# Kernel optimization log

Measured on AMD Instinct MI355X. Metric: run time of the kernel, lower is better.

The kernel has to match this reference:

```python
import jax, jax.numpy as jnp
import numpy as np

EPS = 1e-5


def setup_inputs() -> dict:
    key = jax.random.key(0)
    ks = jax.random.split(key, 6)
    B, N, F = 8, 8192, 64
    xyzs = jax.random.uniform(ks[0], (B, N, 3), dtype=jnp.float32)
    feats = jax.random.normal(ks[1], (B, N, F), dtype=jnp.float32)
    c_in = 3 + F  # 67
    dims = [(64, c_in), (64, 64), (128, 64)]
    inp = {"xyzs": xyzs, "feats": feats}
    for i, (co, ci) in enumerate(dims, start=1):
        inp[f"w{i}"] = jax.random.normal(ks[1 + i], (co, ci), dtype=jnp.float32) / np.sqrt(ci)
        inp[f"b{i}"] = jnp.zeros((co,), jnp.float32)
        inp[f"g{i}"] = jnp.ones((co,), jnp.float32)
        inp[f"bt{i}"] = jnp.zeros((co,), jnp.float32)
        inp[f"m{i}"] = jnp.zeros((co,), jnp.float32)
        inp[f"v{i}"] = jnp.ones((co,), jnp.float32)
    return inp


def sample_farthest_points(xyz, S):
    # Iterative FPS starting from index 0 (pytorch3d default random_start_point=False).
    B, N, _ = xyz.shape
    barange = jnp.arange(B)

    def step(carry, _):
        mind, last = carry                      # mind: [B,N] min sq-dist to selected set
        lastp = xyz[barange, last]              # [B,3]
        d = jnp.sum((xyz - lastp[:, None, :]) ** 2, -1)
        mind = jnp.minimum(mind, d)
        nxt = jnp.argmax(mind, axis=1).astype(jnp.int32)
        return (mind, nxt), nxt

    init = (jnp.full((B, N), 1e10, xyz.dtype), jnp.zeros((B,), jnp.int32))
    _, rest = jax.lax.scan(step, init, None, length=S - 1)  # [S-1, B]
    idx = jnp.concatenate([jnp.zeros((1, B), jnp.int32), rest], 0).T  # [B,S]
    return xyz[barange[:, None], idx], idx


def ball_query(centers, xyz, K, radius):
    # First-K-in-radius semantics of pytorch3d.ops.ball_query; pad idx with -1,
    # pad gathered points with zeros (masked_gather behavior).
    B, N, _ = xyz.shape
    d2 = (jnp.sum(centers ** 2, -1)[:, :, None]
          + jnp.sum(xyz ** 2, -1)[:, None, :]
          - 2.0 * jnp.einsum('bsd,bnd->bsn', centers, xyz))  # [B,S,N]
    within = d2 <= radius * radius
    skey = jnp.where(within, jnp.arange(N, dtype=jnp.int32), N)
    negvals, idx = jax.lax.top_k(-skey, K)      # K smallest keys = first K in-radius
    valid = (-negvals) < N                       # [B,S,K]
    group_idx = jnp.where(valid, idx, -1)
    gathered = xyz[jnp.arange(B)[:, None, None], jnp.where(valid, idx, 0)]  # [B,S,K,3]
    group_xyz = jnp.where(valid[..., None], gathered, 0.0)
    return group_idx, group_xyz


def _mlp_layer(x, w, b, g, bt, m, v):
    # 1x1 Conv2d over channel axis + BatchNorm (eval stats) + ReLU; x: [B,S,K,Cin]
    y = jnp.einsum('bskc,oc->bsko', x, w) + b
    y = g * (y - m) * jax.lax.rsqrt(v + EPS) + bt
    return jax.nn.relu(y)


def reference(xyzs, feats, w1, b1, g1, bt1, m1, v1,
              w2, b2, g2, bt2, m2, v2, w3, b3, g3, bt3, m3, v3):
    S, K, radius = 2048, 32, 0.2
    B = xyzs.shape[0]
    center_xyzs, _ = sample_farthest_points(xyzs, S)             # [B,S,3]
    group_idxs, group_xyzs = ball_query(center_xyzs, xyzs, K, radius)
    group_xyzs = group_xyzs - center_xyzs[:, :, None, :]          # relative coords
    batch_idxs = jnp.arange(B)[:, None, None]
    gf = feats[batch_idxs, jnp.where(group_idxs < 0, 0, group_idxs)]  # [B,S,K,F]
    gf = jnp.concatenate([group_xyzs, gf], axis=-1)
    gf = gf * (group_idxs != -1)[..., None].astype(gf.dtype)      # zero padded slots
    x = _mlp_layer(gf, w1, b1, g1, bt1, m1, v1)
    x = _mlp_layer(x, w2, b2, g2, bt2, m2, v2)
    x = _mlp_layer(x, w3, b3, g3, bt3, m3, v3)
    center_feats = jnp.max(x, axis=2)                             # max over neighbors
    return center_xyzs, center_feats
```

## Files before the change

kernel.cpp:

```cpp
#include <hip/hip_runtime.h>


#define NPTS 8192
#define SCTR 2048
#define NB   8
#define KNN  32
#define NF   64

typedef float v2f __attribute__((ext_vector_type(2)));

__device__ __forceinline__ v2f fps_sqdist_v2(v2f px, v2f py, v2f pz,
                                             v2f lx, v2f ly, v2f lz) {
#pragma clang fp contract(off)
  v2f dx = px - lx;
  v2f dy = py - ly;
  v2f dz = pz - lz;
  v2f xx = dx * dx;
  v2f yy = dy * dy;
  v2f zz = dz * dz;
  return (xx + yy) + zz;
}

__device__ __forceinline__ float sumsq3(float x, float y, float z) {
#pragma clang fp contract(off)
  return (x * x + y * y) + z * z;
}

__device__ __forceinline__ float bq_d2(float sc, float sx,
                                       float cx, float cy, float cz,
                                       float x, float y, float z) {
#pragma clang fp contract(off)
  float dt = fmaf(cz, z, fmaf(cy, y, cx * x));
  return (sc + sx) - 2.0f * dt;
}

template <int CTRL>
__device__ __forceinline__ unsigned long long kmax_dpp(unsigned long long k) {
  int lo = (int)(unsigned int)(k & 0xFFFFFFFFull);
  int hi = (int)(unsigned int)(k >> 32);
  int slo = __builtin_amdgcn_update_dpp(lo, lo, CTRL, 0xF, 0xF, false);
  int shi = __builtin_amdgcn_update_dpp(hi, hi, CTRL, 0xF, 0xF, false);
  unsigned long long sk =
      ((unsigned long long)(unsigned int)shi << 32) | (unsigned int)slo;
  return sk > k ? sk : k;
}

__global__ __launch_bounds__(256, 1) void fps_transpose_kernel(
    const float* __restrict__ xyzs,
    const float* __restrict__ w1, const float* __restrict__ w2, const float* __restrict__ w3,
    float* __restrict__ centers, float* __restrict__ wT)
{
  const int t = threadIdx.x;
  if (blockIdx.x >= NB) {
    int idx = (blockIdx.x - NB) * 256 + t;
    if (idx < 67*64) {
      int c = idx >> 6, o = idx & 63;
      wT[idx] = w1[o*67 + c];
    } else if (idx < 67*64 + 64*64) {
      int r = idx - 67*64; int c = r >> 6, o = r & 63;
      wT[idx] = w2[o*64 + c];
    } else if (idx < 67*64 + 64*64 + 64*128) {
      int r = idx - (67*64 + 64*64); int c = r >> 7, o = r & 127;
      wT[idx] = w3[o*64 + c];
    }
    return;
  }

  const int b = blockIdx.x;
  const float* xb = xyzs + (size_t)b * NPTS * 3;

  __shared__ float sX[NPTS], sY[NPTS], sZ[NPTS];
  __shared__ unsigned long long redk[2][4];
  __shared__ int hist[SCTR];

  for (int i = t; i < NPTS; i += 256) {
    sX[i] = xb[3*i+0];
    sY[i] = xb[3*i+1];
    sZ[i] = xb[3*i+2];
  }
  if (t == 0) hist[0] = 0;
  __syncthreads();

  const int t4 = 4 * t;

  const float4 xA = *(const float4*)(sX + 0    + t4);
  const float4 yA = *(const float4*)(sY + 0    + t4);
  const float4 zA = *(const float4*)(sZ + 0    + t4);
  const float4 xB = *(const float4*)(sX + 1024 + t4);
  const float4 yB = *(const float4*)(sY + 1024 + t4);
  const float4 zB = *(const float4*)(sZ + 1024 + t4);
  const float4 xC = *(const float4*)(sX + 2048 + t4);
  const float4 yC = *(const float4*)(sY + 2048 + t4);
  const float4 zC = *(const float4*)(sZ + 2048 + t4);
  const float4 xD = *(const float4*)(sX + 3072 + t4);
  const float4 yD = *(const float4*)(sY + 3072 + t4);
  const float4 zD = *(const float4*)(sZ + 3072 + t4);
  const float4 xE = *(const float4*)(sX + 4096 + t4);
  const float4 yE = *(const float4*)(sY + 4096 + t4);
  const float4 zE = *(const float4*)(sZ + 4096 + t4);
  const float4 xF = *(const float4*)(sX + 5120 + t4);
  const float4 yF = *(const float4*)(sY + 5120 + t4);
  const float4 zF = *(const float4*)(sZ + 5120 + t4);
  const float4 xG = *(const float4*)(sX + 6144 + t4);
  const float4 yG = *(const float4*)(sY + 6144 + t4);
  const float4 zG = *(const float4*)(sZ + 6144 + t4);
  const float4 xH = *(const float4*)(sX + 7168 + t4);
  const float4 yH = *(const float4*)(sY + 7168 + t4);
  const float4 zH = *(const float4*)(sZ + 7168 + t4);

  float4 mA = make_float4(1e10f,1e10f,1e10f,1e10f);
  float4 mB = mA, mC = mA, mD = mA, mE = mA, mF = mA, mG = mA, mH = mA;

  float lx = sX[0], ly = sY[0], lz = sZ[0];

#define FPS_QUAD(QX, QY, QZ, MV, QOFF, BV, BG)                                  \
  do {                                                                          \
    v2f d;                                                                      \
    d = fps_sqdist_v2((v2f){QX.x,QX.y}, (v2f){QY.x,QY.y}, (v2f){QZ.x,QZ.y},     \
                      lxv, lyv, lzv);                                           \
    MV.x = fminf(MV.x, d.x); if (MV.x > BV) { BV = MV.x; BG = (QOFF)+t4+0; }    \
    MV.y = fminf(MV.y, d.y); if (MV.y > BV) { BV = MV.y; BG = (QOFF)+t4+1; }    \
    d = fps_sqdist_v2((v2f){QX.z,QX.w}, (v2f){QY.z,QY.w}, (v2f){QZ.z,QZ.w},     \
                      lxv, lyv, lzv);                                           \
    MV.z = fminf(MV.z, d.x); if (MV.z > BV) { BV = MV.z; BG = (QOFF)+t4+2; }    \
    MV.w = fminf(MV.w, d.y); if (MV.w > BV) { BV = MV.w; BG = (QOFF)+t4+3; }    \
  } while (0)

  for (int s = 1; s < SCTR; ++s) {
    float bv0 = -1.0f, bv1 = -1.0f; int bg0 = 0, bg1 = 0;
    {
      v2f lxv = {lx, lx}, lyv = {ly, ly}, lzv = {lz, lz};
      FPS_QUAD(xA, yA, zA, mA, 0,    bv0, bg0);
      FPS_QUAD(xB, yB, zB, mB, 1024, bv0, bg0);
      FPS_QUAD(xC, yC, zC, mC, 2048, bv0, bg0);
      FPS_QUAD(xD, yD, zD, mD, 3072, bv0, bg0);
      FPS_QUAD(xE, yE, zE, mE, 4096, bv1, bg1);
      FPS_QUAD(xF, yF, zF, mF, 5120, bv1, bg1);
      FPS_QUAD(xG, yG, zG, mG, 6144, bv1, bg1);
      FPS_QUAD(xH, yH, zH, mH, 7168, bv1, bg1);
    }
    float bv = bv0; int bg = bg0;
    if (bv1 > bv0) { bv = bv1; bg = bg1; }

    unsigned long long key =
        ((unsigned long long)__float_as_uint(bv) << 13) |
        (unsigned long long)(8191 - bg);

    key = kmax_dpp<0x111>(key);
    key = kmax_dpp<0x112>(key);
    key = kmax_dpp<0x114>(key);
    key = kmax_dpp<0x118>(key);
    key = kmax_dpp<0x142>(key);
    key = kmax_dpp<0x143>(key);

    int pb = s & 1;
    if ((t & 63) == 63) redk[pb][t >> 6] = key;
    __syncthreads();

    unsigned long long k4 = redk[pb][t & 3];
    k4 = kmax_dpp<0xB1>(k4);
    k4 = kmax_dpp<0x4E>(k4);

    int i0 = 8191 - (int)(k4 & 0x1FFFull);
    lx = sX[i0]; ly = sY[i0]; lz = sZ[i0];
    if (t == 0) hist[s] = i0;
  }
#undef FPS_QUAD
  __syncthreads();

  for (int s = t; s < SCTR; s += 256) {
    int i = hist[s];
    float* o = centers + ((size_t)b * SCTR + s) * 3;
    o[0] = sX[i]; o[1] = sY[i]; o[2] = sZ[i];
  }
}

__global__ __launch_bounds__(64) void sa_fused_kernel(
    const float* __restrict__ xyzs, const float* __restrict__ feats,
    const float* centers, const float* __restrict__ wT,
    const float* __restrict__ b1, const float* __restrict__ g1, const float* __restrict__ bt1,
    const float* __restrict__ m1, const float* __restrict__ v1,
    const float* __restrict__ b2, const float* __restrict__ g2, const float* __restrict__ bt2,
    const float* __restrict__ m2, const float* __restrict__ v2,
    const float* __restrict__ b3, const float* __restrict__ g3, const float* __restrict__ bt3,
    const float* __restrict__ m3, const float* __restrict__ v3,
    float* out_feats)
{
  constexpr float R2 = (float)(0.2 * 0.2);
  const int bid  = blockIdx.x;
  const int b    = bid >> 11;
  const int lane = threadIdx.x;
  const float* xb = xyzs + (size_t)b * NPTS * 3;
  const float* cp = centers + (size_t)bid * 3;
  float cx = cp[0], cy = cp[1], cz = cp[2];
  float sc = sumsq3(cx, cy, cz);

  __shared__ int   gidx[KNN];
  __shared__ float in_[32*67];
  __shared__ float y_[32*65];

  int cnt = 0;
  for (int base = 0; base < NPTS && cnt < KNN; base += 64) {
    int n = base + lane;
    float x = xb[n*3+0], y = xb[n*3+1], z = xb[n*3+2];
    float sx = sumsq3(x, y, z);
    float d2 = bq_d2(sc, sx, cx, cy, cz, x, y, z);
    bool within = (d2 <= R2);
    unsigned long long mk = __ballot(within);
    int rank = __popcll(mk & ((1ull << lane) - 1ull));
    int slot = cnt + rank;
    if (within && slot < KNN) gidx[slot] = n;
    cnt += (int)__popcll(mk);
  }
  if (cnt > KNN) cnt = KNN;
  __syncthreads();

#pragma unroll 4
  for (int k = 0; k < KNN; ++k) {
    int gk = (k < cnt) ? gidx[k] : -1;
    float fv = 0.f, xv = 0.f;
    if (gk >= 0) {
      fv = feats[((size_t)b * NPTS + gk) * NF + lane];
      if (lane < 3) xv = xb[gk*3 + lane] - cp[lane];
    }
    in_[k*67 + 3 + lane] = fv;
    if (lane < 3) in_[k*67 + lane] = xv;
  }
  __syncthreads();

  const int g = lane >> 3;
  const int h = lane & 7;
  const float* w1T = wT;
  const float* w2T = wT + 67*64;
  const float* w3T = wT + 67*64 + 64*64;

  {
    float acc[4][8];
#pragma unroll
    for (int i=0;i<4;++i)
#pragma unroll
      for (int j=0;j<8;++j) acc[i][j]=0.f;
#pragma unroll 4
    for (int c = 0; c < 67; ++c) {
      float a0 = in_[(4*g+0)*67 + c];
      float a1 = in_[(4*g+1)*67 + c];
      float a2 = in_[(4*g+2)*67 + c];
      float a3 = in_[(4*g+3)*67 + c];
      const float* wr = w1T + c*64 + 8*h;
      float4 wv0 = *(const float4*)(wr);
      float4 wv1 = *(const float4*)(wr + 4);
      float wj[8] = {wv0.x,wv0.y,wv0.z,wv0.w,wv1.x,wv1.y,wv1.z,wv1.w};
#pragma unroll
      for (int j=0;j<8;++j) {
        acc[0][j] = fmaf(a0, wj[j], acc[0][j]);
        acc[1][j] = fmaf(a1, wj[j], acc[1][j]);
        acc[2][j] = fmaf(a2, wj[j], acc[2][j]);
        acc[3][j] = fmaf(a3, wj[j], acc[3][j]);
      }
    }
    float scl[8], shf[8];
#pragma unroll
    for (int j=0;j<8;++j) {
      int o = 8*h + j;
      float r = g1[o] * rsqrtf(v1[o] + 1e-5f);
      scl[j] = r;
      shf[j] = (b1[o] - m1[o]) * r + bt1[o];
    }
#pragma unroll
    for (int i=0;i<4;++i) {
      int k = 4*g + i;
#pragma unroll
      for (int j=0;j<8;++j)
        y_[k*65 + 8*h + j] = fmaxf(fmaf(acc[i][j], scl[j], shf[j]), 0.f);
    }
  }
  __syncthreads();

  {
    float acc[4][8];
#pragma unroll
    for (int i=0;i<4;++i)
#pragma unroll
      for (int j=0;j<8;++j) acc[i][j]=0.f;
#pragma unroll 4
    for (int c = 0; c < 64; ++c) {
      float a0 = y_[(4*g+0)*65 + c];
      float a1 = y_[(4*g+1)*65 + c];
      float a2 = y_[(4*g+2)*65 + c];
      float a3 = y_[(4*g+3)*65 + c];
      const float* wr = w2T + c*64 + 8*h;
      float4 wv0 = *(const float4*)(wr);
      float4 wv1 = *(const float4*)(wr + 4);
      float wj[8] = {wv0.x,wv0.y,wv0.z,wv0.w,wv1.x,wv1.y,wv1.z,wv1.w};
#pragma unroll
      for (int j=0;j<8;++j) {
        acc[0][j] = fmaf(a0, wj[j], acc[0][j]);
        acc[1][j] = fmaf(a1, wj[j], acc[1][j]);
        acc[2][j] = fmaf(a2, wj[j], acc[2][j]);
        acc[3][j] = fmaf(a3, wj[j], acc[3][j]);
      }
    }
    float scl[8], shf[8];
#pragma unroll
    for (int j=0;j<8;++j) {
      int o = 8*h + j;
      float r = g2[o] * rsqrtf(v2[o] + 1e-5f);
      scl[j] = r;
      shf[j] = (b2[o] - m2[o]) * r + bt2[o];
    }
    __syncthreads();
#pragma unroll
    for (int i=0;i<4;++i) {
      int k = 4*g + i;
#pragma unroll
      for (int j=0;j<8;++j)
        in_[k*65 + 8*h + j] = fmaxf(fmaf(acc[i][j], scl[j], shf[j]), 0.f);
    }
  }
  __syncthreads();

  for (int p = 0; p < 2; ++p) {
    float acc[4][8];
#pragma unroll
    for (int i=0;i<4;++i)
#pragma unroll
      for (int j=0;j<8;++j) acc[i][j]=0.f;
#pragma unroll 4
    for (int c = 0; c < 64; ++c) {
      float a0 = in_[(4*g+0)*65 + c];
      float a1 = in_[(4*g+1)*65 + c];
      float a2 = in_[(4*g+2)*65 + c];
      float a3 = in_[(4*g+3)*65 + c];
      const float* wr = w3T + c*128 + p*64 + 8*h;
      float4 wv0 = *(const float4*)(wr);
      float4 wv1 = *(const float4*)(wr + 4);
      float wj[8] = {wv0.x,wv0.y,wv0.z,wv0.w,wv1.x,wv1.y,wv1.z,wv1.w};
#pragma unroll
      for (int j=0;j<8;++j) {
        acc[0][j] = fmaf(a0, wj[j], acc[0][j]);
        acc[1][j] = fmaf(a1, wj[j], acc[1][j]);
        acc[2][j] = fmaf(a2, wj[j], acc[2][j]);
        acc[3][j] = fmaf(a3, wj[j], acc[3][j]);
      }
    }
    float scl[8], shf[8];
#pragma unroll
    for (int j=0;j<8;++j) {
      int o = p*64 + 8*h + j;
      float r = g3[o] * rsqrtf(v3[o] + 1e-5f);
      scl[j] = r;
      shf[j] = (b3[o] - m3[o]) * r + bt3[o];
    }
    float vm[8];
#pragma unroll
    for (int j=0;j<8;++j) {
      float q0 = fmaxf(fmaf(acc[0][j], scl[j], shf[j]), 0.f);
      float q1 = fmaxf(fmaf(acc[1][j], scl[j], shf[j]), 0.f);
      float q2 = fmaxf(fmaf(acc[2][j], scl[j], shf[j]), 0.f);
      float q3 = fmaxf(fmaf(acc[3][j], scl[j], shf[j]), 0.f);
      vm[j] = fmaxf(fmaxf(q0,q1), fmaxf(q2,q3));
    }
#pragma unroll
    for (int mk = 8; mk < 64; mk <<= 1) {
#pragma unroll
      for (int j=0;j<8;++j) vm[j] = fmaxf(vm[j], __shfl_xor(vm[j], mk));
    }
    if (g == 0) {
      float* dst = out_feats + (size_t)bid*128 + p*64 + 8*h;
      *(float4*)dst       = make_float4(vm[0],vm[1],vm[2],vm[3]);
      *(float4*)(dst + 4) = make_float4(vm[4],vm[5],vm[6],vm[7]);
    }
  }
}

extern "C" void kernel_launch(void* const* d_in, const int* in_sizes, int n_in,
                              void* d_out, int out_size, void* d_ws, size_t ws_size,
                              hipStream_t stream) {
  const float* xyzs  = (const float*)d_in[0];
  const float* feats = (const float*)d_in[1];
  const float* w1  = (const float*)d_in[2];
  const float* b1  = (const float*)d_in[3];
  const float* g1  = (const float*)d_in[4];
  const float* bt1 = (const float*)d_in[5];
  const float* m1  = (const float*)d_in[6];
  const float* v1  = (const float*)d_in[7];
  const float* w2  = (const float*)d_in[8];
  const float* b2  = (const float*)d_in[9];
  const float* g2  = (const float*)d_in[10];
  const float* bt2 = (const float*)d_in[11];
  const float* m2  = (const float*)d_in[12];
  const float* v2  = (const float*)d_in[13];
  const float* w3  = (const float*)d_in[14];
  const float* b3  = (const float*)d_in[15];
  const float* g3  = (const float*)d_in[16];
  const float* bt3 = (const float*)d_in[17];
  const float* m3  = (const float*)d_in[18];
  const float* v3  = (const float*)d_in[19];

  float* out       = (float*)d_out;
  float* centers   = out;
  float* out_feats = out + (size_t)NB * SCTR * 3;
  float* wT        = (float*)d_ws;

  hipLaunchKernelGGL(fps_transpose_kernel, dim3(NB + 65), dim3(256), 0, stream,
                     xyzs, w1, w2, w3, centers, wT);
  hipLaunchKernelGGL(sa_fused_kernel, dim3(NB * SCTR), dim3(64), 0, stream,
                     xyzs, feats, centers, wT,
                     b1, g1, bt1, m1, v1,
                     b2, g2, bt2, m2, v2,
                     b3, g3, bt3, m3, v3,
                     out_feats);
}
```

Baseline: 2.362 ms.

## Split fused MLP across two waves and force packed FP32 ops in FPS

The fused ball-query and MLP kernel now runs 128 threads per center instead of 64. Each wave computes half of the output channels of every layer, and the feature gather is split across the two waves. The FPS distance update is rewritten with inline v_pk_add_f32 and v_pk_mul_f32, adding a negated last point so that packed FP32 instructions are guaranteed. The wider block shortens the per-thread dependent chain and cuts register use, at the cost of both waves running the ball-query scan redundantly; the inline asm also limits what the compiler can schedule.

```diff
diff --git a/kernel.cpp b/kernel.cpp
--- a/kernel.cpp
+++ b/kernel.cpp
@@ -9,16 +9,11 @@
 
 typedef float v2f __attribute__((ext_vector_type(2)));
 
-__device__ __forceinline__ v2f fps_sqdist_v2(v2f px, v2f py, v2f pz,
-                                             v2f lx, v2f ly, v2f lz) {
-#pragma clang fp contract(off)
-  v2f dx = px - lx;
-  v2f dy = py - ly;
-  v2f dz = pz - lz;
-  v2f xx = dx * dx;
-  v2f yy = dy * dy;
-  v2f zz = dz * dz;
-  return (xx + yy) + zz;
+__device__ __forceinline__ v2f pk_add(v2f a, v2f b) {
+  v2f r; asm("v_pk_add_f32 %0, %1, %2" : "=v"(r) : "v"(a), "v"(b)); return r;
+}
+__device__ __forceinline__ v2f pk_mul(v2f a, v2f b) {
+  v2f r; asm("v_pk_mul_f32 %0, %1, %2" : "=v"(r) : "v"(a), "v"(b)); return r;
 }
 
 __device__ __forceinline__ float sumsq3(float x, float y, float z) {
@@ -113,23 +108,30 @@
 
   float lx = sX[0], ly = sY[0], lz = sZ[0];
 
-#define FPS_QUAD(QX, QY, QZ, MV, QOFF, BV, BG)                                  \
-  do {                                                                          \
-    v2f d;                                                                      \
-    d = fps_sqdist_v2((v2f){QX.x,QX.y}, (v2f){QY.x,QY.y}, (v2f){QZ.x,QZ.y},     \
-                      lxv, lyv, lzv);                                           \
-    MV.x = fminf(MV.x, d.x); if (MV.x > BV) { BV = MV.x; BG = (QOFF)+t4+0; }    \
-    MV.y = fminf(MV.y, d.y); if (MV.y > BV) { BV = MV.y; BG = (QOFF)+t4+1; }    \
-    d = fps_sqdist_v2((v2f){QX.z,QX.w}, (v2f){QY.z,QY.w}, (v2f){QZ.z,QZ.w},     \
-                      lxv, lyv, lzv);                                           \
-    MV.z = fminf(MV.z, d.x); if (MV.z > BV) { BV = MV.z; BG = (QOFF)+t4+2; }    \
-    MV.w = fminf(MV.w, d.y); if (MV.w > BV) { BV = MV.w; BG = (QOFF)+t4+3; }    \
+#define FPS_HALF(PX0, PX1, PY0, PY1, PZ0, PZ1, MM0, MM1, I0, I1, BV, BG)     \
+  do {                                                                       \
+    v2f px_ = {PX0, PX1}, py_ = {PY0, PY1}, pz_ = {PZ0, PZ1};               \
+    v2f dx_ = pk_add(px_, nlx);                                              \
+    v2f dy_ = pk_add(py_, nly);                                              \
+    v2f dz_ = pk_add(pz_, nlz);                                              \
+    v2f dd_ = pk_add(pk_add(pk_mul(dx_,dx_), pk_mul(dy_,dy_)),               \
+                     pk_mul(dz_,dz_));                                       \
+    MM0 = fminf(MM0, dd_.x); if (MM0 > BV) { BV = MM0; BG = (I0); }          \
+    MM1 = fminf(MM1, dd_.y); if (MM1 > BV) { BV = MM1; BG = (I1); }          \
+  } while (0)
+
+#define FPS_QUAD(QX, QY, QZ, MV, QOFF, BV, BG)                               \
+  do {                                                                       \
+    FPS_HALF(QX.x, QX.y, QY.x, QY.y, QZ.x, QZ.y, MV.x, MV.y,                 \
+             (QOFF)+t4+0, (QOFF)+t4+1, BV, BG);                              \
+    FPS_HALF(QX.z, QX.w, QY.z, QY.w, QZ.z, QZ.w, MV.z, MV.w,                 \
+             (QOFF)+t4+2, (QOFF)+t4+3, BV, BG);                              \
   } while (0)
 
   for (int s = 1; s < SCTR; ++s) {
     float bv0 = -1.0f, bv1 = -1.0f; int bg0 = 0, bg1 = 0;
     {
-      v2f lxv = {lx, lx}, lyv = {ly, ly}, lzv = {lz, lz};
+      v2f nlx = {-lx, -lx}, nly = {-ly, -ly}, nlz = {-lz, -lz};
       FPS_QUAD(xA, yA, zA, mA, 0,    bv0, bg0);
       FPS_QUAD(xB, yB, zB, mB, 1024, bv0, bg0);
       FPS_QUAD(xC, yC, zC, mC, 2048, bv0, bg0);
@@ -166,6 +168,7 @@
     if (t == 0) hist[s] = i0;
   }
 #undef FPS_QUAD
+#undef FPS_HALF
   __syncthreads();
 
   for (int s = t; s < SCTR; s += 256) {
@@ -175,7 +178,7 @@
   }
 }
 
-__global__ __launch_bounds__(64) void sa_fused_kernel(
+__global__ __launch_bounds__(128) void sa_fused_kernel(
     const float* __restrict__ xyzs, const float* __restrict__ feats,
     const float* centers, const float* __restrict__ wT,
     const float* __restrict__ b1, const float* __restrict__ g1, const float* __restrict__ bt1,
@@ -189,7 +192,9 @@
   constexpr float R2 = (float)(0.2 * 0.2);
   const int bid  = blockIdx.x;
   const int b    = bid >> 11;
-  const int lane = threadIdx.x;
+  const int tid  = threadIdx.x;
+  const int w    = tid >> 6;
+  const int lane = tid & 63;
   const float* xb = xyzs + (size_t)b * NPTS * 3;
   const float* cp = centers + (size_t)bid * 3;
   float cx = cp[0], cy = cp[1], cz = cp[2];
@@ -216,7 +221,8 @@
   __syncthreads();
 
 #pragma unroll 4
-  for (int k = 0; k < KNN; ++k) {
+  for (int k2 = 0; k2 < 16; ++k2) {
+    int k = 2*k2 + w;
     int gk = (k < cnt) ? gidx[k] : -1;
     float fv = 0.f, xv = 0.f;
     if (gk >= 0) {
@@ -235,33 +241,31 @@
   const float* w3T = wT + 67*64 + 64*64;
 
   {
-    float acc[4][8];
+    float acc[4][4];
 #pragma unroll
     for (int i=0;i<4;++i)
 #pragma unroll
-      for (int j=0;j<8;++j) acc[i][j]=0.f;
+      for (int j=0;j<4;++j) acc[i][j]=0.f;
 #pragma unroll 4
     for (int c = 0; c < 67; ++c) {
       float a0 = in_[(4*g+0)*67 + c];
       float a1 = in_[(4*g+1)*67 + c];
       float a2 = in_[(4*g+2)*67 + c];
       float a3 = in_[(4*g+3)*67 + c];
-      const float* wr = w1T + c*64 + 8*h;
-      float4 wv0 = *(const float4*)(wr);
-      float4 wv1 = *(const float4*)(wr + 4);
-      float wj[8] = {wv0.x,wv0.y,wv0.z,wv0.w,wv1.x,wv1.y,wv1.z,wv1.w};
-#pragma unroll
-      for (int j=0;j<8;++j) {
+      float4 wv = *(const float4*)(w1T + c*64 + w*32 + 4*h);
+      float wj[4] = {wv.x, wv.y, wv.z, wv.w};
+#pragma unroll
+      for (int j=0;j<4;++j) {
         acc[0][j] = fmaf(a0, wj[j], acc[0][j]);
         acc[1][j] = fmaf(a1, wj[j], acc[1][j]);
         acc[2][j] = fmaf(a2, wj[j], acc[2][j]);
         acc[3][j] = fmaf(a3, wj[j], acc[3][j]);
       }
     }
-    float scl[8], shf[8];
-#pragma unroll
-    for (int j=0;j<8;++j) {
-      int o = 8*h + j;
+    float scl[4], shf[4];
+#pragma unroll
+    for (int j=0;j<4;++j) {
+      int o = w*32 + 4*h + j;
       float r = g1[o] * rsqrtf(v1[o] + 1e-5f);
       scl[j] = r;
       shf[j] = (b1[o] - m1[o]) * r + bt1[o];
@@ -270,40 +274,38 @@
     for (int i=0;i<4;++i) {
       int k = 4*g + i;
 #pragma unroll
-      for (int j=0;j<8;++j)
-        y_[k*65 + 8*h + j] = fmaxf(fmaf(acc[i][j], scl[j], shf[j]), 0.f);
+      for (int j=0;j<4;++j)
+        y_[k*65 + w*32 + 4*h + j] = fmaxf(fmaf(acc[i][j], scl[j], shf[j]), 0.f);
     }
   }
   __syncthreads();
 
   {
-    float acc[4][8];
+    float acc[4][4];
 #pragma unroll
     for (int i=0;i<4;++i)
 #pragma unroll
-      for (int j=0;j<8;++j) acc[i][j]=0.f;
+      for (int j=0;j<4;++j) acc[i][j]=0.f;
 #pragma unroll 4
     for (int c = 0; c < 64; ++c) {
       float a0 = y_[(4*g+0)*65 + c];
       float a1 = y_[(4*g+1)*65 + c];
       float a2 = y_[(4*g+2)*65 + c];
       float a3 = y_[(4*g+3)*65 + c];
-      const float* wr = w2T + c*64 + 8*h;
-      float4 wv0 = *(const float4*)(wr);
-      float4 wv1 = *(const float4*)(wr + 4);
-      float wj[8] = {wv0.x,wv0.y,wv0.z,wv0.w,wv1.x,wv1.y,wv1.z,wv1.w};
-#pragma unroll
-      for (int j=0;j<8;++j) {
+      float4 wv = *(const float4*)(w2T + c*64 + w*32 + 4*h);
+      float wj[4] = {wv.x, wv.y, wv.z, wv.w};
+#pragma unroll
+      for (int j=0;j<4;++j) {
         acc[0][j] = fmaf(a0, wj[j], acc[0][j]);
         acc[1][j] = fmaf(a1, wj[j], acc[1][j]);
         acc[2][j] = fmaf(a2, wj[j], acc[2][j]);
         acc[3][j] = fmaf(a3, wj[j], acc[3][j]);
       }
     }
-    float scl[8], shf[8];
-#pragma unroll
-    for (int j=0;j<8;++j) {
-      int o = 8*h + j;
+    float scl[4], shf[4];
+#pragma unroll
+    for (int j=0;j<4;++j) {
+      int o = w*32 + 4*h + j;
       float r = g2[o] * rsqrtf(v2[o] + 1e-5f);
       scl[j] = r;
       shf[j] = (b2[o] - m2[o]) * r + bt2[o];
@@ -313,47 +315,45 @@
     for (int i=0;i<4;++i) {
       int k = 4*g + i;
 #pragma unroll
-      for (int j=0;j<8;++j)
-        in_[k*65 + 8*h + j] = fmaxf(fmaf(acc[i][j], scl[j], shf[j]), 0.f);
+      for (int j=0;j<4;++j)
+        in_[k*65 + w*32 + 4*h + j] = fmaxf(fmaf(acc[i][j], scl[j], shf[j]), 0.f);
     }
   }
   __syncthreads();
 
   for (int p = 0; p < 2; ++p) {
-    float acc[4][8];
+    float acc[4][4];
 #pragma unroll
     for (int i=0;i<4;++i)
 #pragma unroll
-      for (int j=0;j<8;++j) acc[i][j]=0.f;
+      for (int j=0;j<4;++j) acc[i][j]=0.f;
 #pragma unroll 4
     for (int c = 0; c < 64; ++c) {
       float a0 = in_[(4*g+0)*65 + c];
       float a1 = in_[(4*g+1)*65 + c];
       float a2 = in_[(4*g+2)*65 + c];
       float a3 = in_[(4*g+3)*65 + c];
-      const float* wr = w3T + c*128 + p*64 + 8*h;
-      float4 wv0 = *(const float4*)(wr);
-      float4 wv1 = *(const float4*)(wr + 4);
-      float wj[8] = {wv0.x,wv0.y,wv0.z,wv0.w,wv1.x,wv1.y,wv1.z,wv1.w};
-#pragma unroll
-      for (int j=0;j<8;++j) {
+      float4 wv = *(const float4*)(w3T + c*128 + w*64 + p*32 + 4*h);
+      float wj[4] = {wv.x, wv.y, wv.z, wv.w};
+#pragma unroll
+      for (int j=0;j<4;++j) {
         acc[0][j] = fmaf(a0, wj[j], acc[0][j]);
         acc[1][j] = fmaf(a1, wj[j], acc[1][j]);
         acc[2][j] = fmaf(a2, wj[j], acc[2][j]);
         acc[3][j] = fmaf(a3, wj[j], acc[3][j]);
       }
     }
-    float scl[8], shf[8];
-#pragma unroll
-    for (int j=0;j<8;++j) {
-      int o = p*64 + 8*h + j;
+    float scl[4], shf[4];
+#pragma unroll
+    for (int j=0;j<4;++j) {
+      int o = w*64 + p*32 + 4*h + j;
       float r = g3[o] * rsqrtf(v3[o] + 1e-5f);
       scl[j] = r;
       shf[j] = (b3[o] - m3[o]) * r + bt3[o];
     }
-    float vm[8];
-#pragma unroll
-    for (int j=0;j<8;++j) {
+    float vm[4];
+#pragma unroll
+    for (int j=0;j<4;++j) {
       float q0 = fmaxf(fmaf(acc[0][j], scl[j], shf[j]), 0.f);
       float q1 = fmaxf(fmaf(acc[1][j], scl[j], shf[j]), 0.f);
       float q2 = fmaxf(fmaf(acc[2][j], scl[j], shf[j]), 0.f);
@@ -363,12 +363,11 @@
 #pragma unroll
     for (int mk = 8; mk < 64; mk <<= 1) {
 #pragma unroll
-      for (int j=0;j<8;++j) vm[j] = fmaxf(vm[j], __shfl_xor(vm[j], mk));
+      for (int j=0;j<4;++j) vm[j] = fmaxf(vm[j], __shfl_xor(vm[j], mk));
     }
     if (g == 0) {
-      float* dst = out_feats + (size_t)bid*128 + p*64 + 8*h;
-      *(float4*)dst       = make_float4(vm[0],vm[1],vm[2],vm[3]);
-      *(float4*)(dst + 4) = make_float4(vm[4],vm[5],vm[6],vm[7]);
+      float* dst = out_feats + (size_t)bid*128 + w*64 + p*32 + 4*h;
+      *(float4*)dst = make_float4(vm[0], vm[1], vm[2], vm[3]);
     }
   }
 }
@@ -404,7 +403,7 @@
 
   hipLaunchKernelGGL(fps_transpose_kernel, dim3(NB + 65), dim3(256), 0, stream,
                      xyzs, w1, w2, w3, centers, wT);
-  hipLaunchKernelGGL(sa_fused_kernel, dim3(NB * SCTR), dim3(64), 0, stream,
+  hipLaunchKernelGGL(sa_fused_kernel, dim3(NB * SCTR), dim3(128), 0, stream,
                      xyzs, feats, centers, wT,
                      b1, g1, bt1, m1, v1,
                      b2, g2, bt2, m2, v2,
```

New measurement: 2.389 ms. About the same (+1.2%).
